# Optimization experiments

Measured on AMD Instinct MI355X. Metric: run time of the kernel, lower is better.

Reference implementation:

```python
import jax, jax.numpy as jnp
import numpy as np

B, T, C, H = 2048, 128, 256, 64

def setup_inputs() -> dict:
    key = jax.random.key(0)
    kx, kk, kq, kv = jax.random.split(key, 4)
    s = 1.0 / np.sqrt(C)  # nn.Linear default init scale (approx)
    return {
        "x": jax.random.normal(kx, (B, T, C), dtype=jnp.float32),
        "Wk": jax.random.uniform(kk, (C, H), jnp.float32, -s, s),
        "Wq": jax.random.uniform(kq, (C, H), jnp.float32, -s, s),
        "Wv": jax.random.uniform(kv, (C, H), jnp.float32, -s, s),
    }

def reference(x, Wk, Wq, Wv):
    # x: [B,T,C]; projections to [B,T,H]
    k = jnp.einsum('btc,ch->bth', x, Wk)
    q = jnp.einsum('btc,ch->bth', x, Wq)
    v = jnp.einsum('btc,ch->bth', x, Wv)
    # NOTE: original scales by C**-0.5 (input dim), not head_size**-0.5
    scale = jnp.asarray(C, x.dtype) ** -0.5
    wei = jnp.einsum('bth,bsh->bts', q, k) * scale  # [B,T,T]
    causal = jnp.tril(jnp.ones((T, T), dtype=bool))
    wei = jnp.where(causal, wei, -jnp.inf)
    wei = jax.nn.softmax(wei, axis=-1)
    # dropout is identity in eval mode (deterministic reference)
    return jnp.einsum('bts,bsh->bth', wei, v)
```

## Files before the change

kernel.cpp:

```cpp
#include <hip/hip_runtime.h>

typedef __bf16 bf16;
typedef __bf16 bf16x4 __attribute__((ext_vector_type(4)));
typedef __bf16 bf16x8 __attribute__((ext_vector_type(8)));
typedef float  f32x4  __attribute__((ext_vector_type(4)));

#define B_ 2048
#define T_ 128
#define C_ 256
#define H_ 64

#define SMEM_BYTES 67584

__global__ void wt_kernel(const float* __restrict__ Wk, const float* __restrict__ Wq,
                          const float* __restrict__ Wv, bf16* __restrict__ Wt) {
    int o = blockIdx.x * 256 + threadIdx.x;
    int slot = o >> 14;
    int r    = o & 16383;
    int cc   = r >> 6;
    int h    = r & 63;
    const float* src = (slot == 0) ? Wq : (slot == 1 ? Wk : Wv);
    Wt[slot * 16384 + h * 256 + cc] = (bf16)src[r];
}

__global__ void __launch_bounds__(256, 2)
attn_kernel(const float* __restrict__ xg, const bf16* __restrict__ Wt,
            float* __restrict__ outg) {
    __shared__ __align__(16) char smem_raw[SMEM_BYTES];
    bf16* xs  = (bf16*)smem_raw;
    bf16* Qs  = (bf16*)smem_raw;
    bf16* Ks  = (bf16*)(smem_raw + 18432);
    bf16* Vt  = (bf16*)(smem_raw + 36864);
    bf16* Ps  = (bf16*)smem_raw;
    float* Of = (float*)smem_raw;

    const int tid  = threadIdx.x;
    const int b    = blockIdx.x;
    const int w    = tid >> 6;
    const int lane = tid & 63;
    const int quad = lane >> 4;
    const int n16  = lane & 15;

    const f32x4 zero4 = {0.f, 0.f, 0.f, 0.f};
    const float*  xb  = xg + (size_t)b * (T_ * C_);
    const ushort* WtU = (const ushort*)Wt;

    {
        float4 xa[8], xb4[8];
        #pragma unroll
        for (int i = 0; i < 8; i++) {
            int f = i * 256 + tid;
            xa[i] = *(const float4*)(xb + (f >> 6) * C_ + (f & 63) * 4);
        }
        #pragma unroll
        for (int g = 0; g < 4; g++) {
            float4* cur = (g & 1) ? xb4 : xa;
            float4* nxt = (g & 1) ? xa : xb4;
            if (g < 3) {
                #pragma unroll
                for (int i = 0; i < 8; i++) {
                    int f = (g + 1) * 2048 + i * 256 + tid;
                    nxt[i] = *(const float4*)(xb + (f >> 6) * C_ + (f & 63) * 4);
                }
            }
            #pragma unroll
            for (int i = 0; i < 8; i++) {
                int f = g * 2048 + i * 256 + tid;
                int t = f >> 6, c4 = (f & 63) * 4;
                bf16x4 bv = {(bf16)cur[i].x, (bf16)cur[i].y, (bf16)cur[i].z, (bf16)cur[i].w};
                *(bf16x4*)(xs + t * 264 + c4) = bv;
            }
        }
    }
    __syncthreads();

    f32x4 acc[2][12];
    #pragma unroll
    for (int mt = 0; mt < 2; mt++)
        #pragma unroll
        for (int nt = 0; nt < 12; nt++) acc[mt][nt] = zero4;

    #pragma unroll
    for (int ks = 0; ks < 8; ks++) {
        bf16x8 a[2];
        #pragma unroll
        for (int mt = 0; mt < 2; mt++)
            a[mt] = *(const bf16x8*)(xs + (16 * (2 * w + mt) + n16) * 264 + ks * 32 + 8 * quad);
        #pragma unroll
        for (int nt = 0; nt < 12; nt++) {
            const ushort* wp = WtU + (nt >> 2) * 16384 + (16 * (nt & 3) + n16) * 256 + ks * 32 + 8 * quad;
            bf16x8 bfr = *(const bf16x8*)wp;
            acc[0][nt] = __builtin_amdgcn_mfma_f32_16x16x32_bf16(a[0], bfr, acc[0][nt], 0, 0, 0);
            acc[1][nt] = __builtin_amdgcn_mfma_f32_16x16x32_bf16(a[1], bfr, acc[1][nt], 0, 0, 0);
        }
    }
    __syncthreads();

    #pragma unroll
    for (int mt = 0; mt < 2; mt++) {
        int tbase = 16 * (2 * w + mt) + 4 * quad;
        #pragma unroll
        for (int nt = 0; nt < 8; nt++) {
            bf16* dst = (nt < 4) ? Qs : Ks;
            int h = 16 * (nt & 3) + n16;
            #pragma unroll
            for (int r = 0; r < 4; r++)
                dst[(tbase + r) * 72 + h] = (bf16)acc[mt][nt][r];
        }
        #pragma unroll
        for (int nt = 8; nt < 12; nt++) {
            int h = 16 * (nt - 8) + n16;
            bf16x4 pv = {(bf16)acc[mt][nt][0], (bf16)acc[mt][nt][1],
                         (bf16)acc[mt][nt][2], (bf16)acc[mt][nt][3]};
            *(bf16x4*)(Vt + h * 136 + tbase) = pv;
        }
    }
    __syncthreads();

    f32x4 sacc[2][8];
    int mts[2] = {w, 7 - w};
    #pragma unroll
    for (int half = 0; half < 2; half++) {
        int mt = mts[half];
        int sT = ((mt >> 1) + 1) * 2;
        bf16x8 qa[2];
        #pragma unroll
        for (int ks = 0; ks < 2; ks++)
            qa[ks] = *(const bf16x8*)(Qs + (16 * mt + n16) * 72 + 32 * ks + 8 * quad);
        #pragma unroll
        for (int nt = 0; nt < 8; nt++) {
            sacc[half][nt] = zero4;
            if (nt < sT) {
                bf16x8 kb0 = *(const bf16x8*)(Ks + (16 * nt + n16) * 72 + 8 * quad);
                bf16x8 kb1 = *(const bf16x8*)(Ks + (16 * nt + n16) * 72 + 32 + 8 * quad);
                sacc[half][nt] = __builtin_amdgcn_mfma_f32_16x16x32_bf16(qa[0], kb0, sacc[half][nt], 0, 0, 0);
                sacc[half][nt] = __builtin_amdgcn_mfma_f32_16x16x32_bf16(qa[1], kb1, sacc[half][nt], 0, 0, 0);
            }
        }
        #pragma unroll
        for (int r = 0; r < 4; r++) {
            int t = 16 * mt + 4 * quad + r;
            float mx = -3.0e38f;
            #pragma unroll
            for (int nt = 0; nt < 8; nt++) {
                if (nt < sT) {
                    float v = sacc[half][nt][r] * 0.0625f;
                    v = (16 * nt + n16 <= t) ? v : -3.0e38f;
                    sacc[half][nt][r] = v;
                    mx = fmaxf(mx, v);
                }
            }
            mx = fmaxf(mx, __shfl_xor(mx, 1));
            mx = fmaxf(mx, __shfl_xor(mx, 2));
            mx = fmaxf(mx, __shfl_xor(mx, 4));
            mx = fmaxf(mx, __shfl_xor(mx, 8));
            float sum = 0.f;
            #pragma unroll
            for (int nt = 0; nt < 8; nt++) {
                if (nt < sT) {
                    float p = __builtin_amdgcn_exp2f((sacc[half][nt][r] - mx) * 1.4426950408889634f);
                    sacc[half][nt][r] = p;
                    sum += p;
                }
            }
            sum += __shfl_xor(sum, 1);
            sum += __shfl_xor(sum, 2);
            sum += __shfl_xor(sum, 4);
            sum += __shfl_xor(sum, 8);
            float rinv = 1.0f / sum;
            #pragma unroll
            for (int nt = 0; nt < 8; nt++)
                if (nt < sT) sacc[half][nt][r] *= rinv;
        }
    }
    __syncthreads();

    #pragma unroll
    for (int half = 0; half < 2; half++) {
        int mt = mts[half];
        int sT = ((mt >> 1) + 1) * 2;
        #pragma unroll
        for (int nt = 0; nt < 8; nt++) {
            if (nt < sT) {
                #pragma unroll
                for (int r = 0; r < 4; r++)
                    Ps[(16 * mt + 4 * quad + r) * 136 + 16 * nt + n16] = (bf16)sacc[half][nt][r];
            }
        }
    }
    __syncthreads();

    f32x4 oacc[2][4];
    #pragma unroll
    for (int half = 0; half < 2; half++) {
        int mt  = mts[half];
        int kst = (mt >> 1) + 1;
        #pragma unroll
        for (int nt = 0; nt < 4; nt++) oacc[half][nt] = zero4;
        #pragma unroll
        for (int ks = 0; ks < 4; ks++) {
            if (ks < kst) {
                bf16x8 pa = *(const bf16x8*)(Ps + (16 * mt + n16) * 136 + 32 * ks + 8 * quad);
                #pragma unroll
                for (int nt = 0; nt < 4; nt++) {
                    bf16x8 vb = *(const bf16x8*)(Vt + (16 * nt + n16) * 136 + 32 * ks + 8 * quad);
                    oacc[half][nt] = __builtin_amdgcn_mfma_f32_16x16x32_bf16(pa, vb, oacc[half][nt], 0, 0, 0);
                }
            }
        }
    }
    __syncthreads();

    #pragma unroll
    for (int half = 0; half < 2; half++) {
        int mt = mts[half];
        #pragma unroll
        for (int nt = 0; nt < 4; nt++)
            #pragma unroll
            for (int r = 0; r < 4; r++)
                Of[(16 * mt + 4 * quad + r) * 68 + 16 * nt + n16] = oacc[half][nt][r];
    }
    __syncthreads();
    #pragma unroll
    for (int i = 0; i < 8; i++) {
        int f = tid + 256 * i;
        int t = f >> 4, h4 = (f & 15) * 4;
        float4 v = *(const float4*)(Of + t * 68 + h4);
        *(float4*)(outg + ((size_t)b * T_ + t) * H_ + h4) = v;
    }
}

extern "C" void kernel_launch(void* const* d_in, const int* in_sizes, int n_in,
                              void* d_out, int out_size, void* d_ws, size_t ws_size,
                              hipStream_t stream) {
    const float* x  = (const float*)d_in[0];
    const float* Wk = (const float*)d_in[1];
    const float* Wq = (const float*)d_in[2];
    const float* Wv = (const float*)d_in[3];
    bf16* Wt = (bf16*)d_ws;
    wt_kernel<<<192, 256, 0, stream>>>(Wk, Wq, Wv, Wt);
    attn_kernel<<<B_, 256, 0, stream>>>(x, Wt, (float*)d_out);
}
```

Measured before the change: 474.6 us.

## Load x fragments directly from global, drop LDS staging, raise occupancy

The kernel now reads x straight from global memory into MFMA A fragments, converting to bf16 in registers, so the xs shared-memory tile and its barrier are gone. The output is written directly from accumulators instead of being staged through LDS, and the softmax scale is folded into Q at store time. Shared memory drops to about 53 KB and launch bounds ask for three blocks per CU. In exchange, the x reads are narrower and less coalesced (two float4 per lane per k-step), output stores are scalar and strided, and the higher occupancy target may limit registers for the 96-float accumulator array. Dropping the barrier after the projection looks safe because Q/K/V occupy the same LDS as before and x no longer shares it.

```diff
diff --git a/kernel.cpp b/kernel.cpp
--- a/kernel.cpp
+++ b/kernel.cpp
@@ -10,7 +10,7 @@
 #define C_ 256
 #define H_ 64
 
-#define SMEM_BYTES 67584
+#define SMEM_BYTES 54272
 
 __global__ void wt_kernel(const float* __restrict__ Wk, const float* __restrict__ Wq,
                           const float* __restrict__ Wv, bf16* __restrict__ Wt) {
@@ -23,16 +23,14 @@
     Wt[slot * 16384 + h * 256 + cc] = (bf16)src[r];
 }
 
-__global__ void __launch_bounds__(256, 2)
+__global__ void __launch_bounds__(256, 3)
 attn_kernel(const float* __restrict__ xg, const bf16* __restrict__ Wt,
             float* __restrict__ outg) {
     __shared__ __align__(16) char smem_raw[SMEM_BYTES];
-    bf16* xs  = (bf16*)smem_raw;
     bf16* Qs  = (bf16*)smem_raw;
     bf16* Ks  = (bf16*)(smem_raw + 18432);
     bf16* Vt  = (bf16*)(smem_raw + 36864);
     bf16* Ps  = (bf16*)smem_raw;
-    float* Of = (float*)smem_raw;
 
     const int tid  = threadIdx.x;
     const int b    = blockIdx.x;
@@ -42,37 +40,8 @@
     const int n16  = lane & 15;
 
     const f32x4 zero4 = {0.f, 0.f, 0.f, 0.f};
-    const float*  xb  = xg + (size_t)b * (T_ * C_);
+    const float*  xbp = xg + (size_t)b * (T_ * C_);
     const ushort* WtU = (const ushort*)Wt;
-
-    {
-        float4 xa[8], xb4[8];
-        #pragma unroll
-        for (int i = 0; i < 8; i++) {
-            int f = i * 256 + tid;
-            xa[i] = *(const float4*)(xb + (f >> 6) * C_ + (f & 63) * 4);
-        }
-        #pragma unroll
-        for (int g = 0; g < 4; g++) {
-            float4* cur = (g & 1) ? xb4 : xa;
-            float4* nxt = (g & 1) ? xa : xb4;
-            if (g < 3) {
-                #pragma unroll
-                for (int i = 0; i < 8; i++) {
-                    int f = (g + 1) * 2048 + i * 256 + tid;
-                    nxt[i] = *(const float4*)(xb + (f >> 6) * C_ + (f & 63) * 4);
-                }
-            }
-            #pragma unroll
-            for (int i = 0; i < 8; i++) {
-                int f = g * 2048 + i * 256 + tid;
-                int t = f >> 6, c4 = (f & 63) * 4;
-                bf16x4 bv = {(bf16)cur[i].x, (bf16)cur[i].y, (bf16)cur[i].z, (bf16)cur[i].w};
-                *(bf16x4*)(xs + t * 264 + c4) = bv;
-            }
-        }
-    }
-    __syncthreads();
 
     f32x4 acc[2][12];
     #pragma unroll
@@ -84,8 +53,14 @@
     for (int ks = 0; ks < 8; ks++) {
         bf16x8 a[2];
         #pragma unroll
-        for (int mt = 0; mt < 2; mt++)
-            a[mt] = *(const bf16x8*)(xs + (16 * (2 * w + mt) + n16) * 264 + ks * 32 + 8 * quad);
+        for (int mt = 0; mt < 2; mt++) {
+            const float* ap = xbp + (16 * (2 * w + mt) + n16) * C_ + ks * 32 + 8 * quad;
+            float4 a0 = *(const float4*)(ap);
+            float4 a1 = *(const float4*)(ap + 4);
+            bf16x8 av = {(bf16)a0.x, (bf16)a0.y, (bf16)a0.z, (bf16)a0.w,
+                         (bf16)a1.x, (bf16)a1.y, (bf16)a1.z, (bf16)a1.w};
+            a[mt] = av;
+        }
         #pragma unroll
         for (int nt = 0; nt < 12; nt++) {
             const ushort* wp = WtU + (nt >> 2) * 16384 + (16 * (nt & 3) + n16) * 256 + ks * 32 + 8 * quad;
@@ -94,18 +69,23 @@
             acc[1][nt] = __builtin_amdgcn_mfma_f32_16x16x32_bf16(a[1], bfr, acc[1][nt], 0, 0, 0);
         }
     }
-    __syncthreads();
 
     #pragma unroll
     for (int mt = 0; mt < 2; mt++) {
         int tbase = 16 * (2 * w + mt) + 4 * quad;
         #pragma unroll
-        for (int nt = 0; nt < 8; nt++) {
-            bf16* dst = (nt < 4) ? Qs : Ks;
+        for (int nt = 0; nt < 4; nt++) {
+            int h = 16 * nt + n16;
+            #pragma unroll
+            for (int r = 0; r < 4; r++)
+                Qs[(tbase + r) * 72 + h] = (bf16)(acc[mt][nt][r] * 0.0625f);
+        }
+        #pragma unroll
+        for (int nt = 4; nt < 8; nt++) {
             int h = 16 * (nt & 3) + n16;
             #pragma unroll
             for (int r = 0; r < 4; r++)
-                dst[(tbase + r) * 72 + h] = (bf16)acc[mt][nt][r];
+                Ks[(tbase + r) * 72 + h] = (bf16)acc[mt][nt][r];
         }
         #pragma unroll
         for (int nt = 8; nt < 12; nt++) {
@@ -144,7 +124,7 @@
             #pragma unroll
             for (int nt = 0; nt < 8; nt++) {
                 if (nt < sT) {
-                    float v = sacc[half][nt][r] * 0.0625f;
+                    float v = sacc[half][nt][r];
                     v = (16 * nt + n16 <= t) ? v : -3.0e38f;
                     sacc[half][nt][r] = v;
                     mx = fmaxf(mx, v);
@@ -209,24 +189,15 @@
             }
         }
     }
-    __syncthreads();
-
     #pragma unroll
     for (int half = 0; half < 2; half++) {
         int mt = mts[half];
+        float* ob = outg + ((size_t)b * T_ + 16 * mt + 4 * quad) * H_;
         #pragma unroll
         for (int nt = 0; nt < 4; nt++)
             #pragma unroll
             for (int r = 0; r < 4; r++)
-                Of[(16 * mt + 4 * quad + r) * 68 + 16 * nt + n16] = oacc[half][nt][r];
-    }
-    __syncthreads();
-    #pragma unroll
-    for (int i = 0; i < 8; i++) {
-        int f = tid + 256 * i;
-        int t = f >> 4, h4 = (f & 15) * 4;
-        float4 v = *(const float4*)(Of + t * 68 + h4);
-        *(float4*)(outg + ((size_t)b * T_ + t) * H_ + h4) = v;
+                ob[r * H_ + 16 * nt + n16] = oacc[half][nt][r];
     }
 }
 
```

New measurement: 500.3 us. +5.4%, slower.

## Repartition QKV projection across waves, fold scale into Q, store output directly

Applied to the files above, without the earlier changes.

The projection GEMM now gives each wave three 16-wide output column groups over all 128 rows, instead of two row tiles over all twelve column groups. Each wave therefore loads only three weight fragments per k-step from global memory rather than twelve, at the cost of reading every x row fragment from LDS. The softmax scale is folded into Q when it is written to LDS, and the LDS paddings are changed. The output is written straight from the MFMA accumulators to global memory, removing the staging buffer and its two barriers, though the resulting stores are narrower and less coalesced.

```diff
diff --git a/kernel.cpp b/kernel.cpp
--- a/kernel.cpp
+++ b/kernel.cpp
@@ -10,6 +10,9 @@
 #define C_ 256
 #define H_ 64
 
+#define LDX 264
+#define LDQ 68
+#define LDV 132
 #define SMEM_BYTES 67584
 
 __global__ void wt_kernel(const float* __restrict__ Wk, const float* __restrict__ Wq,
@@ -29,10 +32,9 @@
     __shared__ __align__(16) char smem_raw[SMEM_BYTES];
     bf16* xs  = (bf16*)smem_raw;
     bf16* Qs  = (bf16*)smem_raw;
-    bf16* Ks  = (bf16*)(smem_raw + 18432);
-    bf16* Vt  = (bf16*)(smem_raw + 36864);
+    bf16* Ks  = (bf16*)(smem_raw + 17408);
+    bf16* Vt  = (bf16*)(smem_raw + 34816);
     bf16* Ps  = (bf16*)smem_raw;
-    float* Of = (float*)smem_raw;
 
     const int tid  = threadIdx.x;
     const int b    = blockIdx.x;
@@ -42,7 +44,7 @@
     const int n16  = lane & 15;
 
     const f32x4 zero4 = {0.f, 0.f, 0.f, 0.f};
-    const float*  xb  = xg + (size_t)b * (T_ * C_);
+    const float*  xbp = xg + (size_t)b * (T_ * C_);
     const ushort* WtU = (const ushort*)Wt;
 
     {
@@ -50,7 +52,7 @@
         #pragma unroll
         for (int i = 0; i < 8; i++) {
             int f = i * 256 + tid;
-            xa[i] = *(const float4*)(xb + (f >> 6) * C_ + (f & 63) * 4);
+            xa[i] = *(const float4*)(xbp + (f >> 6) * C_ + (f & 63) * 4);
         }
         #pragma unroll
         for (int g = 0; g < 4; g++) {
@@ -60,7 +62,7 @@
                 #pragma unroll
                 for (int i = 0; i < 8; i++) {
                     int f = (g + 1) * 2048 + i * 256 + tid;
-                    nxt[i] = *(const float4*)(xb + (f >> 6) * C_ + (f & 63) * 4);
+                    nxt[i] = *(const float4*)(xbp + (f >> 6) * C_ + (f & 63) * 4);
                 }
             }
             #pragma unroll
@@ -68,51 +70,67 @@
                 int f = g * 2048 + i * 256 + tid;
                 int t = f >> 6, c4 = (f & 63) * 4;
                 bf16x4 bv = {(bf16)cur[i].x, (bf16)cur[i].y, (bf16)cur[i].z, (bf16)cur[i].w};
-                *(bf16x4*)(xs + t * 264 + c4) = bv;
-            }
-        }
-    }
-    __syncthreads();
-
-    f32x4 acc[2][12];
-    #pragma unroll
-    for (int mt = 0; mt < 2; mt++)
-        #pragma unroll
-        for (int nt = 0; nt < 12; nt++) acc[mt][nt] = zero4;
+                *(bf16x4*)(xs + t * LDX + c4) = bv;
+            }
+        }
+    }
+    __syncthreads();
+
+    const int w3 = 3 * w;
+    const ushort* wb0 = WtU + ((w3 + 0) >> 2) * 16384 + (16 * ((w3 + 0) & 3) + n16) * 256 + 8 * quad;
+    const ushort* wb1 = WtU + ((w3 + 1) >> 2) * 16384 + (16 * ((w3 + 1) & 3) + n16) * 256 + 8 * quad;
+    const ushort* wb2 = WtU + ((w3 + 2) >> 2) * 16384 + (16 * ((w3 + 2) & 3) + n16) * 256 + 8 * quad;
+
+    f32x4 acc[8][3];
+    #pragma unroll
+    for (int mt = 0; mt < 8; mt++)
+        #pragma unroll
+        for (int j = 0; j < 3; j++) acc[mt][j] = zero4;
 
     #pragma unroll
     for (int ks = 0; ks < 8; ks++) {
-        bf16x8 a[2];
-        #pragma unroll
-        for (int mt = 0; mt < 2; mt++)
-            a[mt] = *(const bf16x8*)(xs + (16 * (2 * w + mt) + n16) * 264 + ks * 32 + 8 * quad);
-        #pragma unroll
-        for (int nt = 0; nt < 12; nt++) {
-            const ushort* wp = WtU + (nt >> 2) * 16384 + (16 * (nt & 3) + n16) * 256 + ks * 32 + 8 * quad;
-            bf16x8 bfr = *(const bf16x8*)wp;
-            acc[0][nt] = __builtin_amdgcn_mfma_f32_16x16x32_bf16(a[0], bfr, acc[0][nt], 0, 0, 0);
-            acc[1][nt] = __builtin_amdgcn_mfma_f32_16x16x32_bf16(a[1], bfr, acc[1][nt], 0, 0, 0);
-        }
-    }
-    __syncthreads();
-
-    #pragma unroll
-    for (int mt = 0; mt < 2; mt++) {
-        int tbase = 16 * (2 * w + mt) + 4 * quad;
-        #pragma unroll
-        for (int nt = 0; nt < 8; nt++) {
-            bf16* dst = (nt < 4) ? Qs : Ks;
-            int h = 16 * (nt & 3) + n16;
-            #pragma unroll
-            for (int r = 0; r < 4; r++)
-                dst[(tbase + r) * 72 + h] = (bf16)acc[mt][nt][r];
-        }
-        #pragma unroll
-        for (int nt = 8; nt < 12; nt++) {
-            int h = 16 * (nt - 8) + n16;
-            bf16x4 pv = {(bf16)acc[mt][nt][0], (bf16)acc[mt][nt][1],
-                         (bf16)acc[mt][nt][2], (bf16)acc[mt][nt][3]};
-            *(bf16x4*)(Vt + h * 136 + tbase) = pv;
+        bf16x8 b0 = *(const bf16x8*)(wb0 + ks * 32);
+        bf16x8 b1 = *(const bf16x8*)(wb1 + ks * 32);
+        bf16x8 b2 = *(const bf16x8*)(wb2 + ks * 32);
+        #pragma unroll
+        for (int mt = 0; mt < 8; mt++) {
+            bf16x8 a = *(const bf16x8*)(xs + (16 * mt + n16) * LDX + ks * 32 + 8 * quad);
+            acc[mt][0] = __builtin_amdgcn_mfma_f32_16x16x32_bf16(a, b0, acc[mt][0], 0, 0, 0);
+            acc[mt][1] = __builtin_amdgcn_mfma_f32_16x16x32_bf16(a, b1, acc[mt][1], 0, 0, 0);
+            acc[mt][2] = __builtin_amdgcn_mfma_f32_16x16x32_bf16(a, b2, acc[mt][2], 0, 0, 0);
+        }
+    }
+    __syncthreads();
+
+    #pragma unroll
+    for (int j = 0; j < 3; j++) {
+        int ng = w3 + j;
+        if (ng < 4) {
+            int h = 16 * ng + n16;
+            #pragma unroll
+            for (int mt = 0; mt < 8; mt++) {
+                int tbase = 16 * mt + 4 * quad;
+                #pragma unroll
+                for (int r = 0; r < 4; r++)
+                    Qs[(tbase + r) * LDQ + h] = (bf16)(acc[mt][j][r] * 0.0625f);
+            }
+        } else if (ng < 8) {
+            int h = 16 * (ng - 4) + n16;
+            #pragma unroll
+            for (int mt = 0; mt < 8; mt++) {
+                int tbase = 16 * mt + 4 * quad;
+                #pragma unroll
+                for (int r = 0; r < 4; r++)
+                    Ks[(tbase + r) * LDQ + h] = (bf16)acc[mt][j][r];
+            }
+        } else {
+            int h = 16 * (ng - 8) + n16;
+            #pragma unroll
+            for (int mt = 0; mt < 8; mt++) {
+                bf16x4 pv = {(bf16)acc[mt][j][0], (bf16)acc[mt][j][1],
+                             (bf16)acc[mt][j][2], (bf16)acc[mt][j][3]};
+                *(bf16x4*)(Vt + h * LDV + 16 * mt + 4 * quad) = pv;
+            }
         }
     }
     __syncthreads();
@@ -126,13 +144,13 @@
         bf16x8 qa[2];
         #pragma unroll
         for (int ks = 0; ks < 2; ks++)
-            qa[ks] = *(const bf16x8*)(Qs + (16 * mt + n16) * 72 + 32 * ks + 8 * quad);
+            qa[ks] = *(const bf16x8*)(Qs + (16 * mt + n16) * LDQ + 32 * ks + 8 * quad);
         #pragma unroll
         for (int nt = 0; nt < 8; nt++) {
             sacc[half][nt] = zero4;
             if (nt < sT) {
-                bf16x8 kb0 = *(const bf16x8*)(Ks + (16 * nt + n16) * 72 + 8 * quad);
-                bf16x8 kb1 = *(const bf16x8*)(Ks + (16 * nt + n16) * 72 + 32 + 8 * quad);
+                bf16x8 kb0 = *(const bf16x8*)(Ks + (16 * nt + n16) * LDQ + 8 * quad);
+                bf16x8 kb1 = *(const bf16x8*)(Ks + (16 * nt + n16) * LDQ + 32 + 8 * quad);
                 sacc[half][nt] = __builtin_amdgcn_mfma_f32_16x16x32_bf16(qa[0], kb0, sacc[half][nt], 0, 0, 0);
                 sacc[half][nt] = __builtin_amdgcn_mfma_f32_16x16x32_bf16(qa[1], kb1, sacc[half][nt], 0, 0, 0);
             }
@@ -144,7 +162,7 @@
             #pragma unroll
             for (int nt = 0; nt < 8; nt++) {
                 if (nt < sT) {
-                    float v = sacc[half][nt][r] * 0.0625f;
+                    float v = sacc[half][nt][r];
                     v = (16 * nt + n16 <= t) ? v : -3.0e38f;
                     sacc[half][nt][r] = v;
                     mx = fmaxf(mx, v);
@@ -184,49 +202,36 @@
             if (nt < sT) {
                 #pragma unroll
                 for (int r = 0; r < 4; r++)
-                    Ps[(16 * mt + 4 * quad + r) * 136 + 16 * nt + n16] = (bf16)sacc[half][nt][r];
-            }
-        }
-    }
-    __syncthreads();
-
-    f32x4 oacc[2][4];
+                    Ps[(16 * mt + 4 * quad + r) * LDV + 16 * nt + n16] = (bf16)sacc[half][nt][r];
+            }
+        }
+    }
+    __syncthreads();
+
     #pragma unroll
     for (int half = 0; half < 2; half++) {
         int mt  = mts[half];
         int kst = (mt >> 1) + 1;
-        #pragma unroll
-        for (int nt = 0; nt < 4; nt++) oacc[half][nt] = zero4;
+        f32x4 oacc[4];
+        #pragma unroll
+        for (int nt = 0; nt < 4; nt++) oacc[nt] = zero4;
         #pragma unroll
         for (int ks = 0; ks < 4; ks++) {
             if (ks < kst) {
-                bf16x8 pa = *(const bf16x8*)(Ps + (16 * mt + n16) * 136 + 32 * ks + 8 * quad);
+                bf16x8 pa = *(const bf16x8*)(Ps + (16 * mt + n16) * LDV + 32 * ks + 8 * quad);
                 #pragma unroll
                 for (int nt = 0; nt < 4; nt++) {
-                    bf16x8 vb = *(const bf16x8*)(Vt + (16 * nt + n16) * 136 + 32 * ks + 8 * quad);
-                    oacc[half][nt] = __builtin_amdgcn_mfma_f32_16x16x32_bf16(pa, vb, oacc[half][nt], 0, 0, 0);
-                }
-            }
-        }
-    }
-    __syncthreads();
-
-    #pragma unroll
-    for (int half = 0; half < 2; half++) {
-        int mt = mts[half];
-        #pragma unroll
-        for (int nt = 0; nt < 4; nt++)
-            #pragma unroll
-            for (int r = 0; r < 4; r++)
-                Of[(16 * mt + 4 * quad + r) * 68 + 16 * nt + n16] = oacc[half][nt][r];
-    }
-    __syncthreads();
-    #pragma unroll
-    for (int i = 0; i < 8; i++) {
-        int f = tid + 256 * i;
-        int t = f >> 4, h4 = (f & 15) * 4;
-        float4 v = *(const float4*)(Of + t * 68 + h4);
-        *(float4*)(outg + ((size_t)b * T_ + t) * H_ + h4) = v;
+                    bf16x8 vb = *(const bf16x8*)(Vt + (16 * nt + n16) * LDV + 32 * ks + 8 * quad);
+                    oacc[nt] = __builtin_amdgcn_mfma_f32_16x16x32_bf16(pa, vb, oacc[nt], 0, 0, 0);
+                }
+            }
+        }
+        float* ob = outg + ((size_t)b * T_ + 16 * mt + 4 * quad) * H_;
+        #pragma unroll
+        for (int r = 0; r < 4; r++)
+            #pragma unroll
+            for (int nt = 0; nt < 4; nt++)
+                ob[r * H_ + 16 * nt + n16] = oacc[nt][r];
     }
 }
 
```

Measured after the change: 433.8 us. -8.6%, faster.
